# Kernel tuning notes

Hardware: AMD Instinct MI355X
Metric: run time of the kernel (lower is better)

Reference implementation:

```python
import jax, jax.numpy as jnp
import numpy as np

N_NODES = 50000
N_EDGES = 600000
D = 128
N_LAYERS = 4  # 2 base + 2 resnet layers
N_GRAPHS = 64
NEG_SLOPE = 0.01  # F.leaky_relu default


def setup_inputs() -> dict:
    key = jax.random.key(0)
    k1, k2, k3, k4, k5 = jax.random.split(key, 5)
    x = jax.random.normal(k1, (N_NODES, D), dtype=jnp.float32)
    edge_index = jax.random.randint(k2, (2, N_EDGES), 0, N_NODES, dtype=jnp.int64)
    batch = jnp.sort(jax.random.randint(k3, (N_NODES,), 0, N_GRAPHS, dtype=jnp.int64))
    Wl = jax.random.normal(k4, (N_LAYERS, D, D), dtype=jnp.float32) * 0.05
    bl = jnp.zeros((N_LAYERS, D), dtype=jnp.float32)
    Wr = jax.random.normal(k5, (N_LAYERS, D, D), dtype=jnp.float32) * 0.05
    return {"x": x, "edge_index": edge_index, "batch": batch,
            "Wl": Wl, "bl": bl, "Wr": Wr}


def _mean_aggregate(x, src, dst, n_nodes):
    # mean over incoming neighbors; isolated nodes get 0 (PyG scatter-mean semantics)
    s = jax.ops.segment_sum(x[src], dst, num_segments=n_nodes)  # [N, D]
    cnt = jax.ops.segment_sum(jnp.ones((src.shape[0],), x.dtype), dst,
                              num_segments=n_nodes)
    return s / jnp.maximum(cnt, 1.0)[:, None]


def reference(x, edge_index, batch, Wl, bl, Wr):
    src, dst = edge_index[0], edge_index[1]
    n = x.shape[0]
    for i in range(N_LAYERS):
        agg = _mean_aggregate(x, src, dst, n)                      # [N, D]
        # SAGEConv: lin_l(agg) + lin_r(x); lin_l has bias, lin_r does not
        x_new = agg @ Wl[i].T + bl[i] + x @ Wr[i].T
        x_new = jnp.where(x_new >= 0, x_new, NEG_SLOPE * x_new)    # leaky_relu
        x = x_new if i < 2 else x + x_new                          # residual after first 2
    # global mean pool per graph
    pooled = jax.ops.segment_sum(x, batch, num_segments=N_GRAPHS)  # [G, D]
    counts = jax.ops.segment_sum(jnp.ones((n,), x.dtype), batch,
                                 num_segments=N_GRAPHS)
    return pooled / jnp.maximum(counts, 1.0)[:, None]
```

## Files before the change

### kernel.cpp

```cpp
#include <hip/hip_runtime.h>

#define N_NODES 50000
#define N_EDGES 600000
#define DIM 128
#define N_LAYERS 4
#define N_GRAPHS 64
#define NEG_SLOPE 0.01f
#define NB_SCAN ((N_NODES + 255) / 256)
#define NB_CNT ((N_EDGES + 255) / 256)
#define NC_CONV (N_NODES * DIM / 8 / 256)
#define NB_PACK 64
#define RS 264

typedef __attribute__((ext_vector_type(8))) short short8;
typedef __attribute__((ext_vector_type(16))) float floatx16;

__device__ __forceinline__ unsigned short f2bf(float f) {
    union { float f; unsigned u; } c; c.f = f;
    unsigned u = c.u;
    unsigned r = (u + 0x7FFFu + ((u >> 16) & 1u)) >> 16;
    return (unsigned short)r;
}
__device__ __forceinline__ float bfraw2f(unsigned short b) {
    union { unsigned u; float f; } c; c.u = ((unsigned)b) << 16;
    return c.f;
}
__device__ __forceinline__ float bflo(unsigned u) {
    union { unsigned u; float f; } c; c.u = u << 16; return c.f;
}
__device__ __forceinline__ float bfhi(unsigned u) {
    union { unsigned u; float f; } c; c.u = u & 0xFFFF0000u; return c.f;
}

__global__ void zero2(int* a, int na, int* b, int nb) {
    int i = blockIdx.x * blockDim.x + threadIdx.x;
    if (i < na) a[i] = 0;
    else if (i < na + nb) b[i - na] = 0;
}

__global__ void preprocess(const float4* __restrict__ x, uint4* __restrict__ xb,
                           const float* __restrict__ Wl, const float* __restrict__ Wr,
                           ushort* __restrict__ wpk,
                           const int* __restrict__ edst, int* __restrict__ deg) {
    int b = blockIdx.x;
    if (b < NC_CONV) {
        int i = b * 256 + threadIdx.x;
        float4 a = x[i * 2], c = x[i * 2 + 1];
        uint4 o;
        o.x = ((unsigned)f2bf(a.y) << 16) | f2bf(a.x);
        o.y = ((unsigned)f2bf(a.w) << 16) | f2bf(a.z);
        o.z = ((unsigned)f2bf(c.y) << 16) | f2bf(c.x);
        o.w = ((unsigned)f2bf(c.w) << 16) | f2bf(c.z);
        xb[i] = o;
    } else if (b < NC_CONV + NB_PACK) {
        int u = (b - NC_CONV) * 4 + (threadIdx.x >> 6);
        int l = threadIdx.x & 63;
        int layer = u >> 6, m = (u >> 5) & 1, s = (u >> 2) & 7, tt = u & 3;
        const float* W = ((m == 0) ? Wl : Wr) + (size_t)layer * DIM * DIM;
        int n = tt * 32 + (l & 31);
        int kb = s * 16 + (l >> 5) * 8;
        size_t off = ((size_t)u * 64 + l) * 8;
        for (int j = 0; j < 8; j++)
            wpk[off + j] = f2bf(W[n * DIM + kb + j]);
    } else {
        int e = (b - NC_CONV - NB_PACK) * 256 + threadIdx.x;
        if (e < N_EDGES) atomicAdd(&deg[edst[e]], 1);
    }
}

__global__ void scan_pass1(const int* __restrict__ deg, int* __restrict__ bsum) {
    int i = blockIdx.x * 256 + threadIdx.x;
    int v = (i < N_NODES) ? deg[i] : 0;
    for (int off = 32; off > 0; off >>= 1) v += __shfl_down(v, off, 64);
    __shared__ int ws[4];
    int lane = threadIdx.x & 63, w = threadIdx.x >> 6;
    if (lane == 0) ws[w] = v;
    __syncthreads();
    if (threadIdx.x == 0) bsum[blockIdx.x] = ws[0] + ws[1] + ws[2] + ws[3];
}

__global__ void scan_pass2(int* __restrict__ bsum) {
    __shared__ int sm[256];
    int t = threadIdx.x;
    int v = (t < NB_SCAN) ? bsum[t] : 0;
    sm[t] = v;
    __syncthreads();
    for (int off = 1; off < 256; off <<= 1) {
        int u = (t >= off) ? sm[t - off] : 0;
        __syncthreads();
        sm[t] += u;
        __syncthreads();
    }
    if (t < NB_SCAN) bsum[t] = sm[t] - v;
}

__global__ void scan_pass3(const int* __restrict__ deg, const int* __restrict__ bsum,
                           int* __restrict__ rp) {
    int i = blockIdx.x * 256 + threadIdx.x;
    int v = (i < N_NODES) ? deg[i] : 0;
    int lane = threadIdx.x & 63, w = threadIdx.x >> 6;
    int s = v;
    for (int off = 1; off < 64; off <<= 1) {
        int t = __shfl_up(s, off, 64);
        if (lane >= off) s += t;
    }
    __shared__ int ws[4];
    if (lane == 63) ws[w] = s;
    __syncthreads();
    int wo = 0;
    for (int k = 0; k < 4; k++) wo += (k < w) ? ws[k] : 0;
    int incl = s + wo + bsum[blockIdx.x];
    if (i < N_NODES) rp[i + 1] = incl;
    if (i == 0) rp[0] = 0;
}

__global__ void fill_gstart(const int* __restrict__ src, const int* __restrict__ dst,
                            const int* __restrict__ rp, int* __restrict__ fill,
                            int* __restrict__ csr,
                            const int* __restrict__ batch, int* __restrict__ gstart) {
    int b = blockIdx.x;
    if (b < NB_CNT) {
        int e = b * 256 + threadIdx.x;
        if (e >= N_EDGES) return;
        int d = dst[e];
        int pos = atomicAdd(&fill[d], 1);
        csr[rp[d] + pos] = src[e];
    } else {
        int i = (b - NB_CNT) * 256 + threadIdx.x;
        if (i >= N_NODES) return;
        int g0 = batch[i];
        if (i == 0) {
            for (int g = 0; g <= g0; g++) gstart[g] = 0;
        } else {
            int p = batch[i - 1];
            for (int g = p + 1; g <= g0; g++) gstart[g] = i;
        }
        if (i == N_NODES - 1) {
            for (int g = g0 + 1; g <= N_GRAPHS; g++) gstart[g] = N_NODES;
        }
    }
}

__global__ __launch_bounds__(256) void agg_mean_wave4(const uint4* __restrict__ x16B,
                                                      const int* __restrict__ rp,
                                                      const int* __restrict__ csr,
                                                      uint4* __restrict__ agg16B) {
    int wv = threadIdx.x >> 6, lane = threadIdx.x & 63;
    int node = blockIdx.x * 4 + wv;
    if (node >= N_NODES) return;
    int s = rp[node], e = rp[node + 1];
    int ll = lane & 15, eg = lane >> 4;
    float a0 = 0.f, a1 = 0.f, a2 = 0.f, a3 = 0.f, a4 = 0.f, a5 = 0.f, a6 = 0.f, a7 = 0.f;
    for (int base = s; base < e; base += 64) {
        int cnt = min(64, e - base);
        unsigned myidx = (base + lane < e) ? (unsigned)csr[base + lane] : 0u;
        for (int j = 0; j < cnt; j += 16) {
            uint4 v[4];
#pragma unroll
            for (int k = 0; k < 4; k++) {
                int sel = j + k * 4 + eg;
                unsigned idx = __shfl(myidx, sel, 64);
                v[k] = make_uint4(0u, 0u, 0u, 0u);
                if (sel < cnt) v[k] = x16B[(size_t)idx * 16 + ll];
            }
#pragma unroll
            for (int k = 0; k < 4; k++) {
                a0 += bflo(v[k].x); a1 += bfhi(v[k].x);
                a2 += bflo(v[k].y); a3 += bfhi(v[k].y);
                a4 += bflo(v[k].z); a5 += bfhi(v[k].z);
                a6 += bflo(v[k].w); a7 += bfhi(v[k].w);
            }
        }
    }
    a0 += __shfl_xor(a0, 16, 64); a0 += __shfl_xor(a0, 32, 64);
    a1 += __shfl_xor(a1, 16, 64); a1 += __shfl_xor(a1, 32, 64);
    a2 += __shfl_xor(a2, 16, 64); a2 += __shfl_xor(a2, 32, 64);
    a3 += __shfl_xor(a3, 16, 64); a3 += __shfl_xor(a3, 32, 64);
    a4 += __shfl_xor(a4, 16, 64); a4 += __shfl_xor(a4, 32, 64);
    a5 += __shfl_xor(a5, 16, 64); a5 += __shfl_xor(a5, 32, 64);
    a6 += __shfl_xor(a6, 16, 64); a6 += __shfl_xor(a6, 32, 64);
    a7 += __shfl_xor(a7, 16, 64); a7 += __shfl_xor(a7, 32, 64);
    if (eg == 0) {
        float inv = 1.0f / (float)max(e - s, 1);
        uint4 o;
        o.x = ((unsigned)f2bf(a1 * inv) << 16) | f2bf(a0 * inv);
        o.y = ((unsigned)f2bf(a3 * inv) << 16) | f2bf(a2 * inv);
        o.z = ((unsigned)f2bf(a5 * inv) << 16) | f2bf(a4 * inv);
        o.w = ((unsigned)f2bf(a7 * inv) << 16) | f2bf(a6 * inv);
        agg16B[(size_t)node * 16 + ll] = o;
    }
}

__global__ __launch_bounds__(256, 4) void fused_layer_mfma(const ushort* __restrict__ agg,
                                                           const ushort* __restrict__ xin,
                                                           ushort* __restrict__ xout,
                                                           const ushort* __restrict__ wpk,
                                                           const float* __restrict__ bias,
                                                           int residual) {
    __shared__ ushort sA[64 * RS];
    int t = threadIdx.x;
    int node0 = blockIdx.x * 64;

    const uint4* aggv = (const uint4*)(agg + (size_t)node0 * DIM);
    const uint4* xv   = (const uint4*)(xin + (size_t)node0 * DIM);
    for (int i = t; i < 64 * 32; i += 256) {
        int r = i >> 5, c = i & 31;
        uint4 val = make_uint4(0u, 0u, 0u, 0u);
        if (node0 + r < N_NODES)
            val = (c < 16) ? aggv[r * 16 + c] : xv[r * 16 + (c - 16)];
        *(uint4*)&sA[r * RS + c * 8] = val;
    }
    __syncthreads();

    int w = t >> 6, l = t & 63;
    int m0 = (w >> 1) * 32;
    int th = w & 1;
    const ushort* arow = &sA[(m0 + (l & 31)) * RS];
    int khalf = (l >> 5) * 8;

    floatx16 acc0, acc1;
    for (int ii = 0; ii < 16; ii++) acc0[ii] = acc1[ii] = 0.f;

    const ushort* wl8 = wpk + (size_t)l * 8 + (size_t)(2 * th) * 512;
#pragma unroll
    for (int s2 = 0; s2 < 16; s2++) {
        int m = s2 >> 3, s = s2 & 7;
        short8 a = *(const short8*)(arow + m * 128 + s * 16 + khalf);
        size_t fb = (size_t)((m * 8 + s) * 4) * 512;
        short8 b0 = *(const short8*)(wl8 + fb);
        short8 b1 = *(const short8*)(wl8 + fb + 512);
        acc0 = __builtin_amdgcn_mfma_f32_32x32x16_bf16(a, b0, acc0, 0, 0, 0);
        acc1 = __builtin_amdgcn_mfma_f32_32x32x16_bf16(a, b1, acc1, 0, 0, 0);
    }

    int col = l & 31;
    int rbase = 4 * (l >> 5);
    floatx16 accs[2] = {acc0, acc1};
    for (int ti = 0; ti < 2; ti++) {
        int n = (2 * th + ti) * 32 + col;
        float bv = bias[n];
#pragma unroll
        for (int r = 0; r < 16; r++) {
            int row = (r & 3) + 8 * (r >> 2) + rbase;
            int gm = m0 + row;
            int gn = node0 + gm;
            if (gn >= N_NODES) continue;
            float v = accs[ti][r] + bv;
            v = (v >= 0.f) ? v : NEG_SLOPE * v;
            if (residual) v += bfraw2f(sA[gm * RS + 128 + n]);
            xout[(size_t)gn * DIM + n] = f2bf(v);
        }
    }
}

__global__ __launch_bounds__(128) void pool_partial(const ushort* __restrict__ xb,
                                                    const int* __restrict__ batch,
                                                    float* __restrict__ pooled) {
    int nb = blockIdx.x * 128;
    int ne = min(nb + 128, N_NODES);
    int d = threadIdx.x;
    int gcur = batch[nb];
    float acc = 0.f;
    for (int n = nb; n < ne; n++) {
        int g = batch[n];
        if (g != gcur) {
            atomicAdd(&pooled[gcur * DIM + d], acc);
            acc = 0.f;
            gcur = g;
        }
        acc += bfraw2f(xb[(size_t)n * DIM + d]);
    }
    atomicAdd(&pooled[gcur * DIM + d], acc);
}

__global__ void pool_final(const float* __restrict__ pooled,
                           const int* __restrict__ gstart,
                           float* __restrict__ out) {
    int i = blockIdx.x * blockDim.x + threadIdx.x;
    if (i >= N_GRAPHS * DIM) return;
    int g = i >> 7;
    int cnt = gstart[g + 1] - gstart[g];
    out[i] = pooled[i] / (float)max(cnt, 1);
}


extern "C" void kernel_launch(void* const* d_in, const int* in_sizes, int n_in,
                              void* d_out, int out_size, void* d_ws, size_t ws_size,
                              hipStream_t stream) {
    const float* x     = (const float*)d_in[0];
    const int*   ei    = (const int*)d_in[1];
    const int*   batch = (const int*)d_in[2];
    const float* Wl    = (const float*)d_in[3];
    const float* bl    = (const float*)d_in[4];
    const float* Wr    = (const float*)d_in[5];
    float* out = (float*)d_out;

    const int* esrc = ei;
    const int* edst = ei + N_EDGES;

    ushort* xb0  = (ushort*)d_ws;
    ushort* xbuf = xb0 + (size_t)N_NODES * DIM;
    ushort* agg  = xbuf + (size_t)N_NODES * DIM;
    ushort* wpk  = agg + (size_t)N_NODES * DIM;
    int* deg    = (int*)(wpk + (size_t)N_LAYERS * 2 * DIM * DIM);
    int* fill   = deg + N_NODES;
    int* csr    = fill + N_NODES;
    int* rp     = csr + N_EDGES;
    int* gstart = rp + (N_NODES + 1);
    int* bsum   = gstart + (N_GRAPHS + 1);
    float* pooled = (float*)(bsum + NB_SCAN);

    zero2<<<(2 * N_NODES + N_GRAPHS * DIM + 255) / 256, 256, 0, stream>>>(
        deg, 2 * N_NODES, (int*)pooled, N_GRAPHS * DIM);

    preprocess<<<NC_CONV + NB_PACK + NB_CNT, 256, 0, stream>>>(
        (const float4*)x, (uint4*)xb0, Wl, Wr, wpk, edst, deg);

    scan_pass1<<<NB_SCAN, 256, 0, stream>>>(deg, bsum);
    scan_pass2<<<1, 256, 0, stream>>>(bsum);
    scan_pass3<<<NB_SCAN, 256, 0, stream>>>(deg, bsum, rp);

    fill_gstart<<<NB_CNT + NB_SCAN, 256, 0, stream>>>(esrc, edst, rp, fill, csr,
                                                      batch, gstart);

    int agg_blocks = (N_NODES + 3) / 4;
    int gemm_blocks = (N_NODES + 63) / 64;
    for (int l = 0; l < N_LAYERS; l++) {
        const ushort* xin = (l == 0) ? xb0 : xbuf;
        agg_mean_wave4<<<agg_blocks, 256, 0, stream>>>((const uint4*)xin, rp, csr, (uint4*)agg);
        fused_layer_mfma<<<gemm_blocks, 256, 0, stream>>>(
            agg, xin, xbuf, wpk + (size_t)l * 2 * DIM * DIM,
            bl + (size_t)l * DIM, (l >= 2) ? 1 : 0);
    }

    pool_partial<<<(N_NODES + 127) / 128, 128, 0, stream>>>(xbuf, batch, pooled);
    pool_final<<<(N_GRAPHS * DIM + 255) / 256, 256, 0, stream>>>(pooled, gstart, out);
}
```

Before: 337.0 us.

## Fuse mean aggregation into the SAGE MFMA layer kernel with ping-pong buffers

Merges the neighbor mean-aggregation kernel into the per-layer GEMM kernel. Each wave gathers and averages neighbors for 16 rows and writes the result straight into shared memory, so the agg buffer is never written to or read back from global memory and one launch per layer goes away. The layer output now alternates between two buffers, since the kernel reads x for neighbor gathers while writing the new x. In exchange, each block serializes 16 gathers per wave and has far fewer independent waves for latency hiding than the old 4-nodes-per-block agg kernel. That can lower memory-level parallelism for the irregular gather.

Measured after the change: 358.5 us. 1.06x slower.

```diff
diff --git a/kernel.cpp b/kernel.cpp
--- a/kernel.cpp
+++ b/kernel.cpp
@@ -141,87 +141,83 @@
     }
 }
 
-__global__ __launch_bounds__(256) void agg_mean_wave4(const uint4* __restrict__ x16B,
-                                                      const int* __restrict__ rp,
-                                                      const int* __restrict__ csr,
-                                                      uint4* __restrict__ agg16B) {
-    int wv = threadIdx.x >> 6, lane = threadIdx.x & 63;
-    int node = blockIdx.x * 4 + wv;
-    if (node >= N_NODES) return;
-    int s = rp[node], e = rp[node + 1];
-    int ll = lane & 15, eg = lane >> 4;
-    float a0 = 0.f, a1 = 0.f, a2 = 0.f, a3 = 0.f, a4 = 0.f, a5 = 0.f, a6 = 0.f, a7 = 0.f;
-    for (int base = s; base < e; base += 64) {
-        int cnt = min(64, e - base);
-        unsigned myidx = (base + lane < e) ? (unsigned)csr[base + lane] : 0u;
-        for (int j = 0; j < cnt; j += 16) {
-            uint4 v[4];
-#pragma unroll
-            for (int k = 0; k < 4; k++) {
-                int sel = j + k * 4 + eg;
-                unsigned idx = __shfl(myidx, sel, 64);
-                v[k] = make_uint4(0u, 0u, 0u, 0u);
-                if (sel < cnt) v[k] = x16B[(size_t)idx * 16 + ll];
-            }
-#pragma unroll
-            for (int k = 0; k < 4; k++) {
-                a0 += bflo(v[k].x); a1 += bfhi(v[k].x);
-                a2 += bflo(v[k].y); a3 += bfhi(v[k].y);
-                a4 += bflo(v[k].z); a5 += bfhi(v[k].z);
-                a6 += bflo(v[k].w); a7 += bfhi(v[k].w);
-            }
-        }
-    }
-    a0 += __shfl_xor(a0, 16, 64); a0 += __shfl_xor(a0, 32, 64);
-    a1 += __shfl_xor(a1, 16, 64); a1 += __shfl_xor(a1, 32, 64);
-    a2 += __shfl_xor(a2, 16, 64); a2 += __shfl_xor(a2, 32, 64);
-    a3 += __shfl_xor(a3, 16, 64); a3 += __shfl_xor(a3, 32, 64);
-    a4 += __shfl_xor(a4, 16, 64); a4 += __shfl_xor(a4, 32, 64);
-    a5 += __shfl_xor(a5, 16, 64); a5 += __shfl_xor(a5, 32, 64);
-    a6 += __shfl_xor(a6, 16, 64); a6 += __shfl_xor(a6, 32, 64);
-    a7 += __shfl_xor(a7, 16, 64); a7 += __shfl_xor(a7, 32, 64);
-    if (eg == 0) {
-        float inv = 1.0f / (float)max(e - s, 1);
-        uint4 o;
-        o.x = ((unsigned)f2bf(a1 * inv) << 16) | f2bf(a0 * inv);
-        o.y = ((unsigned)f2bf(a3 * inv) << 16) | f2bf(a2 * inv);
-        o.z = ((unsigned)f2bf(a5 * inv) << 16) | f2bf(a4 * inv);
-        o.w = ((unsigned)f2bf(a7 * inv) << 16) | f2bf(a6 * inv);
-        agg16B[(size_t)node * 16 + ll] = o;
-    }
-}
-
-__global__ __launch_bounds__(256, 4) void fused_layer_mfma(const ushort* __restrict__ agg,
-                                                           const ushort* __restrict__ xin,
-                                                           ushort* __restrict__ xout,
-                                                           const ushort* __restrict__ wpk,
-                                                           const float* __restrict__ bias,
-                                                           int residual) {
+__global__ __launch_bounds__(256, 4) void sage_fused(const uint* __restrict__ x32,
+                                                     ushort* __restrict__ xout,
+                                                     const int* __restrict__ rp,
+                                                     const int* __restrict__ csr,
+                                                     const ushort* __restrict__ wpk,
+                                                     const float* __restrict__ bias,
+                                                     int residual) {
     __shared__ ushort sA[64 * RS];
     int t = threadIdx.x;
+    int w = t >> 6, lane = t & 63;
     int node0 = blockIdx.x * 64;
-
-    const uint4* aggv = (const uint4*)(agg + (size_t)node0 * DIM);
-    const uint4* xv   = (const uint4*)(xin + (size_t)node0 * DIM);
-    for (int i = t; i < 64 * 32; i += 256) {
-        int r = i >> 5, c = i & 31;
-        uint4 val = make_uint4(0u, 0u, 0u, 0u);
-        if (node0 + r < N_NODES)
-            val = (c < 16) ? aggv[r * 16 + c] : xv[r * 16 + (c - 16)];
-        *(uint4*)&sA[r * RS + c * 8] = val;
+    int ll = lane & 15, eg = lane >> 4;
+    const uint4* x16B = (const uint4*)x32;
+
+    for (int i = 0; i < 16; i++) {
+        int r = w * 16 + i;
+        int node = node0 + r;
+        ushort* row = sA + (size_t)r * RS;
+        if (node >= N_NODES) {
+            ((uint*)row)[lane] = 0u;
+            ((uint*)row)[64 + lane] = 0u;
+            continue;
+        }
+        ((uint*)row)[64 + lane] = x32[(size_t)node * 64 + lane];
+        int s = rp[node], e = rp[node + 1];
+        float a0 = 0.f, a1 = 0.f, a2 = 0.f, a3 = 0.f,
+              a4 = 0.f, a5 = 0.f, a6 = 0.f, a7 = 0.f;
+        for (int base = s; base < e; base += 64) {
+            int cnt = min(64, e - base);
+            unsigned myidx = (base + lane < e) ? (unsigned)csr[base + lane] : 0u;
+            for (int j = 0; j < cnt; j += 16) {
+                uint4 v[4];
+#pragma unroll
+                for (int k = 0; k < 4; k++) {
+                    int sel = j + k * 4 + eg;
+                    unsigned idx = __shfl(myidx, sel, 64);
+                    v[k] = make_uint4(0u, 0u, 0u, 0u);
+                    if (sel < cnt) v[k] = x16B[(size_t)idx * 16 + ll];
+                }
+#pragma unroll
+                for (int k = 0; k < 4; k++) {
+                    a0 += bflo(v[k].x); a1 += bfhi(v[k].x);
+                    a2 += bflo(v[k].y); a3 += bfhi(v[k].y);
+                    a4 += bflo(v[k].z); a5 += bfhi(v[k].z);
+                    a6 += bflo(v[k].w); a7 += bfhi(v[k].w);
+                }
+            }
+        }
+        a0 += __shfl_xor(a0, 16, 64); a0 += __shfl_xor(a0, 32, 64);
+        a1 += __shfl_xor(a1, 16, 64); a1 += __shfl_xor(a1, 32, 64);
+        a2 += __shfl_xor(a2, 16, 64); a2 += __shfl_xor(a2, 32, 64);
+        a3 += __shfl_xor(a3, 16, 64); a3 += __shfl_xor(a3, 32, 64);
+        a4 += __shfl_xor(a4, 16, 64); a4 += __shfl_xor(a4, 32, 64);
+        a5 += __shfl_xor(a5, 16, 64); a5 += __shfl_xor(a5, 32, 64);
+        a6 += __shfl_xor(a6, 16, 64); a6 += __shfl_xor(a6, 32, 64);
+        a7 += __shfl_xor(a7, 16, 64); a7 += __shfl_xor(a7, 32, 64);
+        if (eg == 0) {
+            float inv = 1.0f / (float)max(e - s, 1);
+            uint4 o;
+            o.x = ((unsigned)f2bf(a1 * inv) << 16) | f2bf(a0 * inv);
+            o.y = ((unsigned)f2bf(a3 * inv) << 16) | f2bf(a2 * inv);
+            o.z = ((unsigned)f2bf(a5 * inv) << 16) | f2bf(a4 * inv);
+            o.w = ((unsigned)f2bf(a7 * inv) << 16) | f2bf(a6 * inv);
+            ((uint4*)row)[ll] = o;
+        }
     }
     __syncthreads();
 
-    int w = t >> 6, l = t & 63;
     int m0 = (w >> 1) * 32;
     int th = w & 1;
-    const ushort* arow = &sA[(m0 + (l & 31)) * RS];
-    int khalf = (l >> 5) * 8;
+    const ushort* arow = &sA[(m0 + (lane & 31)) * RS];
+    int khalf = (lane >> 5) * 8;
 
     floatx16 acc0, acc1;
     for (int ii = 0; ii < 16; ii++) acc0[ii] = acc1[ii] = 0.f;
 
-    const ushort* wl8 = wpk + (size_t)l * 8 + (size_t)(2 * th) * 512;
+    const ushort* wl8 = wpk + (size_t)lane * 8 + (size_t)(2 * th) * 512;
 #pragma unroll
     for (int s2 = 0; s2 < 16; s2++) {
         int m = s2 >> 3, s = s2 & 7;
@@ -233,8 +229,8 @@
         acc1 = __builtin_amdgcn_mfma_f32_32x32x16_bf16(a, b1, acc1, 0, 0, 0);
     }
 
-    int col = l & 31;
-    int rbase = 4 * (l >> 5);
+    int col = lane & 31;
+    int rbase = 4 * (lane >> 5);
     floatx16 accs[2] = {acc0, acc1};
     for (int ti = 0; ti < 2; ti++) {
         int n = (2 * th + ti) * 32 + col;
@@ -298,10 +294,10 @@
     const int* esrc = ei;
     const int* edst = ei + N_EDGES;
 
-    ushort* xb0  = (ushort*)d_ws;
-    ushort* xbuf = xb0 + (size_t)N_NODES * DIM;
-    ushort* agg  = xbuf + (size_t)N_NODES * DIM;
-    ushort* wpk  = agg + (size_t)N_NODES * DIM;
+    ushort* xb0 = (ushort*)d_ws;
+    ushort* xbA = xb0 + (size_t)N_NODES * DIM;
+    ushort* xbB = xbA + (size_t)N_NODES * DIM;
+    ushort* wpk = xbB + (size_t)N_NODES * DIM;
     int* deg    = (int*)(wpk + (size_t)N_LAYERS * 2 * DIM * DIM);
     int* fill   = deg + N_NODES;
     int* csr    = fill + N_NODES;
@@ -323,16 +319,17 @@
     fill_gstart<<<NB_CNT + NB_SCAN, 256, 0, stream>>>(esrc, edst, rp, fill, csr,
                                                       batch, gstart);
 
-    int agg_blocks = (N_NODES + 3) / 4;
-    int gemm_blocks = (N_NODES + 63) / 64;
+    int blocks = (N_NODES + 63) / 64;
+    const ushort* xin = xb0;
+    ushort* xo = xbA;
     for (int l = 0; l < N_LAYERS; l++) {
-        const ushort* xin = (l == 0) ? xb0 : xbuf;
-        agg_mean_wave4<<<agg_blocks, 256, 0, stream>>>((const uint4*)xin, rp, csr, (uint4*)agg);
-        fused_layer_mfma<<<gemm_blocks, 256, 0, stream>>>(
-            agg, xin, xbuf, wpk + (size_t)l * 2 * DIM * DIM,
+        sage_fused<<<blocks, 256, 0, stream>>>(
+            (const uint*)xin, xo, rp, csr, wpk + (size_t)l * 2 * DIM * DIM,
             bl + (size_t)l * DIM, (l >= 2) ? 1 : 0);
-    }
-
-    pool_partial<<<(N_NODES + 127) / 128, 128, 0, stream>>>(xbuf, batch, pooled);
+        xin = xo;
+        xo = (xin == xbA) ? xbB : xbA;
+    }
+
+    pool_partial<<<(N_NODES + 127) / 128, 128, 0, stream>>>(xin, batch, pooled);
     pool_final<<<(N_GRAPHS * DIM + 255) / 256, 256, 0, stream>>>(pooled, gstart, out);
 }
```
